# Optimization experiments

Hardware: AMD Instinct MI355X
Metric: run time of the kernel (lower is better)

Reference implementation:

```python
import jax, jax.numpy as jnp
import numpy as np

N_FFT = 2048
HOP = 441
WIN_SIZE = 7
PAD = WIN_SIZE // 2
NP_WIN = WIN_SIZE * WIN_SIZE
COV_NORM = NP_WIN / (NP_WIN - 1.0)  # sample covariance, skimage default
DATA_RANGE = 2.0  # skimage float dtype_range (-1,1)
C1 = (0.01 * DATA_RANGE) ** 2
C2 = (0.03 * DATA_RANGE) ** 2
EPS = 1e-8

# periodic hann window (librosa fftbins=True)
_HANN = 0.5 - 0.5 * np.cos(2.0 * np.pi * np.arange(N_FFT) / N_FFT)


def wav_to_spectrogram(x):
    # x: [B, C, S] -> magnitude spectrogram [B, C, T, F]
    pad = N_FFT // 2
    xp = jnp.pad(x, ((0, 0), (0, 0), (pad, pad)), mode='reflect')  # torch 'reflect'
    L = xp.shape[-1]
    n_frames = (L - N_FFT) // HOP + 1
    idx = jnp.arange(n_frames)[:, None] * HOP + jnp.arange(N_FFT)[None, :]
    frames = xp[..., idx] * jnp.asarray(_HANN, xp.dtype)  # [B,C,T,N_FFT]
    spec = jnp.fft.rfft(frames, axis=-1)
    mag = jnp.sqrt(jnp.maximum(spec.real ** 2 + spec.imag ** 2, EPS))
    return mag


def _umean_last(x):
    # 1D uniform mean filter (size 7) along last axis, scipy 'reflect' boundary
    xp = jnp.pad(x, [(0, 0)] * (x.ndim - 1) + [(PAD, PAD)], mode='symmetric')
    cs = jnp.cumsum(xp, axis=-1)
    zero = jnp.zeros(cs.shape[:-1] + (1,), cs.dtype)
    cs = jnp.concatenate([zero, cs], axis=-1)
    return (cs[..., WIN_SIZE:] - cs[..., :-WIN_SIZE]) / WIN_SIZE


def umean2d(x):
    # separable 7x7 uniform filter over last two axes
    x = _umean_last(x)
    x = jnp.swapaxes(_umean_last(jnp.swapaxes(x, -1, -2)), -1, -2)
    return x


def ssim_map_mean(X, Y):
    ux, uy = umean2d(X), umean2d(Y)
    uxx, uyy, uxy = umean2d(X * X), umean2d(Y * Y), umean2d(X * Y)
    vx = COV_NORM * (uxx - ux * ux)
    vy = COV_NORM * (uyy - uy * uy)
    vxy = COV_NORM * (uxy - ux * uy)
    S = ((2 * ux * uy + C1) * (2 * vxy + C2)) / ((ux * ux + uy * uy + C1) * (vx + vy + C2))
    # crop pad on each side (skimage) then mean over the spatial map
    return jnp.mean(S[..., PAD:-PAD, PAD:-PAD], axis=(-2, -1))


def setup_inputs() -> dict:
    key = jax.random.key(0)
    k1, k2 = jax.random.split(key)
    B, C, S = 32, 2, 176400
    output = jax.random.normal(k1, (B, C, S), dtype=jnp.float32)
    target = jax.random.normal(k2, (B, C, S), dtype=jnp.float32)
    return {"output": output, "target": target}


def reference(output, target):
    so = wav_to_spectrogram(output)
    st = wav_to_spectrogram(target)
    res = ssim_map_mean(so, st)  # [B, C]
    return res[..., None, None]  # [B, C, 1, 1]
```

## Files before the change

kernel.cpp:

```cpp
#include <hip/hip_runtime.h>
#include <math.h>

#ifndef M_PI
#define M_PI 3.14159265358979323846
#endif

constexpr int S_LEN    = 176400;
constexpr int NFFT     = 2048;
constexpr int NC       = 1024;
constexpr int HOP_     = 441;
constexpr int T_FRAMES = 401;
constexpr int F_BINS   = 1025;
constexpr int F_STRIDE = 1028;
constexpr int N_CH     = 64;
constexpr float EPS_   = 1e-8f;
constexpr float C1_    = 0.0004f;
constexpr float C2_    = 0.0036f;
constexpr float COV_NORM_ = 49.0f / 48.0f;

constexpr int WIN_OFF  = 0;
constexpr int TWG_OFF  = 2048;
constexpr int UTW_OFF  = 3584;
constexpr int SPEC_OFF = 5696;

constexpr int ROWS_PW   = 12;
constexpr int NCHUNKS_R = 33;
constexpr int BANDS     = 5;
constexpr int BAND_ADV  = 248;

typedef float vf2 __attribute__((ext_vector_type(2)));

__device__ __forceinline__ int phys(int i) { return i ^ ((i >> 2) & 15) ^ ((i >> 6) & 15); }

__device__ __forceinline__ vf2 pk_add(vf2 a, vf2 b) {
    vf2 r; asm("v_pk_add_f32 %0, %1, %2" : "=v"(r) : "v"(a), "v"(b)); return r;
}
__device__ __forceinline__ vf2 pk_sub(vf2 a, vf2 b) {
    vf2 r; asm("v_pk_add_f32 %0, %1, %2 neg_lo:[0,1] neg_hi:[0,1]" : "=v"(r) : "v"(a), "v"(b)); return r;
}
__device__ __forceinline__ vf2 pk_sub_i(vf2 b, vf2 d) {
    vf2 r; asm("v_pk_add_f32 %0, %1, %2 op_sel:[0,1] op_sel_hi:[1,0] neg_hi:[0,1]"
               : "=v"(r) : "v"(b), "v"(d)); return r;
}
__device__ __forceinline__ vf2 pk_add_i(vf2 b, vf2 d) {
    vf2 r; asm("v_pk_add_f32 %0, %1, %2 op_sel:[0,1] op_sel_hi:[1,0] neg_lo:[0,1]"
               : "=v"(r) : "v"(b), "v"(d)); return r;
}
__device__ __forceinline__ vf2 pk_cmul(vf2 y, vf2 w) {
    vf2 t, r;
    asm("v_pk_mul_f32 %0, %1, %2 op_sel:[0,0] op_sel_hi:[0,1]"
        : "=v"(t) : "v"(y), "v"(w));
    asm("v_pk_fma_f32 %0, %1, %2, %3 op_sel:[1,1,0] op_sel_hi:[1,0,1] neg_lo:[1,0,0]"
        : "=v"(r) : "v"(y), "v"(w), "v"(t));
    return r;
}

__global__ __launch_bounds__(256) void init_tables_kernel(float* __restrict__ ws, float* __restrict__ out) {
    const int idx = blockIdx.x * 256 + threadIdx.x;
    if (idx < 64) out[idx] = 0.0f;
    if (idx < NFFT) {
        ws[WIN_OFF + idx] = 0.5f - 0.5f * cosf((float)(2.0 * M_PI / NFFT) * (float)idx);
    }
    if (idx < 768) {
        float ang = -2.0f * (float)M_PI * (float)idx / (float)NC;
        float s, c; sincosf(ang, &s, &c);
        ws[TWG_OFF + 2*idx] = c; ws[TWG_OFF + 2*idx+1] = s;
    }
    if (idx < F_BINS) {
        float ang = -(float)M_PI * (float)idx / (float)NC;
        float s, c; sincosf(ang, &s, &c);
        ws[UTW_OFF + 2*idx] = c; ws[UTW_OFF + 2*idx+1] = s;
    }
}

__device__ __forceinline__ void r4_dif_inplace(
    vf2* __restrict__ A, int r0, int r1, int r2, int r3,
    vf2 w1, vf2 w2, vf2 w3, bool tw)
{
    vf2 x0c = A[r0];
    vf2 x1c = A[r1];
    vf2 x2c = A[r2];
    vf2 x3c = A[r3];

    vf2 a = pk_add(x0c, x2c);
    vf2 b = pk_sub(x0c, x2c);
    vf2 c = pk_add(x1c, x3c);
    vf2 d = pk_sub(x1c, x3c);

    vf2 y0 = pk_add(a, c);
    vf2 y2 = pk_sub(a, c);
    vf2 y1 = pk_sub_i(b, d);
    vf2 y3 = pk_add_i(b, d);

    A[r0] = y0;
    A[r1] = tw ? pk_cmul(y1, w1) : y1;
    A[r2] = tw ? pk_cmul(y2, w2) : y2;
    A[r3] = tw ? pk_cmul(y3, w3) : y3;
}

__global__ __launch_bounds__(256, 8) void stft_mag_kernel(
    const float* __restrict__ x0, const float* __restrict__ x1,
    float* __restrict__ ws, int ch0, int chbase, int nlay, int swizzle)
{
    __shared__ vf2 buf[2 * NC];

    const int tid = threadIdx.x;

    int ch, t;
    if (swizzle) {
        int g = blockIdx.x;
        ch = ch0 + (g & 7) * 8 + ((g >> 3) & 7);
        t  = g >> 6;
    } else {
        t  = blockIdx.x;
        ch = ch0 + blockIdx.y;
    }

    const float* __restrict__ xin0 = x0 + (size_t)ch * S_LEN;
    const float* __restrict__ xin1 = x1 + (size_t)ch * S_LEN;
    const float* __restrict__ win  = ws + WIN_OFF;
    const vf2*   __restrict__ twg  = (const vf2*)(ws + TWG_OFF);
    const vf2*   __restrict__ utw  = (const vf2*)(ws + UTW_OFF);

    const int base = t * HOP_ - NFFT / 2;
    float* fA0 = (float*)buf;
    float* fA1 = (float*)(buf + NC);
    if (base >= 0 && base + NFFT <= S_LEN) {
        #pragma unroll
        for (int k = 0; k < NFFT / 256; ++k) {
            int n = k * 256 + tid;
            int j = base + n;
            float w = win[n];
            int p = 2 * phys(n >> 1) + (n & 1);
            fA0[p] = xin0[j] * w;
            fA1[p] = xin1[j] * w;
        }
    } else {
        #pragma unroll
        for (int k = 0; k < NFFT / 256; ++k) {
            int n = k * 256 + tid;
            int j = base + n;
            j = (j < 0) ? -j : j;
            j = (j >= S_LEN) ? (2 * S_LEN - 2 - j) : j;
            float w = win[n];
            int p = 2 * phys(n >> 1) + (n & 1);
            fA0[p] = xin0[j] * w;
            fA1[p] = xin1[j] * w;
        }
    }
    __syncthreads();

    #pragma unroll
    for (int s = 0; s < 5; ++s) {
        const int M  = 256 >> (2 * s);
        const int q  = tid & (M - 1);
        const int e  = q << (2 * s);
        const int i0 = 4 * (tid - q) + q;

        const int r0 = phys(i0);
        const int r1 = phys(i0 + M);
        const int r2 = phys(i0 + 2 * M);
        const int r3 = phys(i0 + 3 * M);

        vf2 w1, w2, w3;
        if (s < 4) {
            w1 = twg[e];
            w2 = twg[2 * e];
            w3 = twg[3 * e];
        } else {
            w1.x = 1.0f; w1.y = 0.0f; w2 = w1; w3 = w1;
        }

        r4_dif_inplace(buf,      r0, r1, r2, r3, w1, w2, w3, s < 4);
        r4_dif_inplace(buf + NC, r0, r1, r2, r3, w1, w2, w3, s < 4);

        __syncthreads();
    }

    const size_t perT = (size_t)T_FRAMES * F_STRIDE;
    float* __restrict__ sout0 =
        ws + SPEC_OFF + (size_t)(ch - chbase) * perT + (size_t)t * F_STRIDE;
    float* __restrict__ sout1 = sout0 + (size_t)nlay * perT;

    const int R8 = ((tid & 3) << 6) | ((tid & 12) << 2) | ((tid >> 2) & 12) | ((tid >> 6) & 3);

    #pragma unroll
    for (int k = 0; k < 5; ++k) {
        int r = k * 256 + tid;
        if (k < 4 || tid == 0) {
            const int ra = (k < 4) ? ((R8 << 2) | k) : 0;
            const int rn = (NC - r) & (NC - 1);
            const int rb = ((rn & 3) << 8) | ((rn & 12) << 4) | (rn & 48)
                         | ((rn >> 4) & 12) | ((rn >> 8) & 3);
            const int ia = phys(ra);
            const int ib = phys(rb);
            vf2 wu = utw[r];

            {
                vf2 Zr = buf[ia];
                vf2 Zn = buf[ib];
                float Ex = 0.5f * (Zr.x + Zn.x);
                float Ey = 0.5f * (Zr.y - Zn.y);
                float Ox = 0.5f * (Zr.y + Zn.y);
                float Oy = 0.5f * (Zn.x - Zr.x);
                float Xx = Ex + wu.x * Ox - wu.y * Oy;
                float Xy = Ey + wu.x * Oy + wu.y * Ox;
                sout0[r] = sqrtf(fmaxf(Xx * Xx + Xy * Xy, EPS_));
            }
            {
                vf2 Zr = buf[NC + ia];
                vf2 Zn = buf[NC + ib];
                float Ex = 0.5f * (Zr.x + Zn.x);
                float Ey = 0.5f * (Zr.y - Zn.y);
                float Ox = 0.5f * (Zr.y + Zn.y);
                float Oy = 0.5f * (Zn.x - Zr.x);
                float Xx = Ex + wu.x * Ox - wu.y * Oy;
                float Xy = Ey + wu.x * Oy + wu.y * Ox;
                sout1[r] = sqrtf(fmaxf(Xx * Xx + Xy * Xy, EPS_));
            }
        }
    }
}

#define HWIN7(sarr, W) {                                                     \
    float p0 = sarr[0], p01 = p0 + sarr[1], p012 = p01 + sarr[2],            \
          P = p012 + sarr[3];                                                \
    float a1 = __shfl_down(p012, 1, 64);                                     \
    float A1 = __shfl_down(P,    1, 64);                                     \
    float b0 = __shfl_down(p0,   2, 64);                                     \
    float b1 = __shfl_down(p01,  2, 64);                                     \
    W[0] = P + a1;                                                           \
    W[1] = P - p0 + A1;                                                      \
    W[2] = W[1] - sarr[1] + b0;                                              \
    W[3] = W[2] - sarr[2] + (b1 - b0);                                       \
}

__global__ __launch_bounds__(256) void ssim_kernel(
    const float* __restrict__ ws, float* __restrict__ out,
    int ch0, int nch)
{
    const int tid  = threadIdx.x;
    const int wid  = blockIdx.x * 4 + (tid >> 6);
    const int lane = tid & 63;
    const int total = nch * BANDS * NCHUNKS_R;
    if (wid >= total) return;

    const int cg    = wid / (BANDS * NCHUNKS_R);
    const int rem   = wid - cg * (BANDS * NCHUNKS_R);
    const int band  = rem / NCHUNKS_R;
    const int chunk = rem - band * NCHUNKS_R;

    const int t0 = 3 + chunk * ROWS_PW;
    const int t1 = min(t0 + ROWS_PW, T_FRAMES - 3);

    const int cb = band * BAND_ADV;
    int c4 = cb + 4 * lane;
    if (c4 > 1024) c4 = 1024;

    const size_t perT = (size_t)T_FRAMES * F_STRIDE;
    const float* __restrict__ X = ws + SPEC_OFF + (size_t)cg * perT + c4;
    const float* __restrict__ Y = ws + SPEC_OFF + ((size_t)nch + cg) * perT + c4;

    const int  fo      = cb + 3 + 4 * lane;
    const bool lane_ok = (lane <= 61);
    const float inv49  = 1.0f / 49.0f;

    float sx[4] = {0,0,0,0}, sy[4] = {0,0,0,0}, sxx[4] = {0,0,0,0},
          syy[4] = {0,0,0,0}, sxy[4] = {0,0,0,0};
    float rgx[6][4], rgy[6][4];

    #pragma unroll
    for (int w = 0; w < 6; ++w) {
        const int rr = t0 - 3 + w;
        float4 xv = *(const float4*)(X + (size_t)rr * F_STRIDE);
        float4 yv = *(const float4*)(Y + (size_t)rr * F_STRIDE);
        float xa[4] = {xv.x, xv.y, xv.z, xv.w}, ya[4] = {yv.x, yv.y, yv.z, yv.w};
        #pragma unroll
        for (int c = 0; c < 4; ++c) {
            sx[c] += xa[c]; sy[c] += ya[c];
            sxx[c] += xa[c]*xa[c]; syy[c] += ya[c]*ya[c]; sxy[c] += xa[c]*ya[c];
            rgx[w][c] = xa[c]; rgy[w][c] = ya[c];
        }
    }

    float4 cxa = *(const float4*)(X + (size_t)(t0 + 3) * F_STRIDE);
    float4 cya = *(const float4*)(Y + (size_t)(t0 + 3) * F_STRIDE);

    double acc = 0.0;

    #pragma unroll 1
    for (int tb = t0; tb < t1; tb += 6) {
        #pragma unroll
        for (int j = 0; j < 6; ++j) {
            const int t = tb + j;
            const int tn = min(t + 4, T_FRAMES - 1);
            float4 nxa = *(const float4*)(X + (size_t)tn * F_STRIDE);
            float4 nya = *(const float4*)(Y + (size_t)tn * F_STRIDE);

            float xa[4] = {cxa.x, cxa.y, cxa.z, cxa.w};
            float ya[4] = {cya.x, cya.y, cya.z, cya.w};

            #pragma unroll
            for (int c = 0; c < 4; ++c) {
                sx[c] += xa[c]; sy[c] += ya[c];
                sxx[c] += xa[c]*xa[c]; syy[c] += ya[c]*ya[c]; sxy[c] += xa[c]*ya[c];
            }

            float wx[4], wy[4], wxx[4], wyy[4], wxy[4];
            HWIN7(sx,  wx);
            HWIN7(sy,  wy);
            HWIN7(sxx, wxx);
            HWIN7(syy, wyy);
            HWIN7(sxy, wxy);

            const bool live = (t < t1);
            #pragma unroll
            for (int c = 0; c < 4; ++c) {
                if (live && lane_ok && (fo + c <= 1021)) {
                    float ux  = wx[c]  * inv49, uy  = wy[c]  * inv49;
                    float uxx = wxx[c] * inv49, uyy = wyy[c] * inv49, uxy = wxy[c] * inv49;
                    float vx  = COV_NORM_ * (uxx - ux * ux);
                    float vy  = COV_NORM_ * (uyy - uy * uy);
                    float vxy = COV_NORM_ * (uxy - ux * uy);
                    float num = (2.f * ux * uy + C1_) * (2.f * vxy + C2_);
                    float den = (ux * ux + uy * uy + C1_) * (vx + vy + C2_);
                    acc += (double)(num * __builtin_amdgcn_rcpf(den));
                }
            }

            #pragma unroll
            for (int c = 0; c < 4; ++c) {
                float bx_ = rgx[j][c], by_ = rgy[j][c];
                sx[c]  -= bx_;      sy[c]  -= by_;
                sxx[c] -= bx_*bx_;  syy[c] -= by_*by_;  sxy[c] -= bx_*by_;
                rgx[j][c] = xa[c];  rgy[j][c] = ya[c];
            }

            cxa = nxa; cya = nya;
        }
    }

    #pragma unroll
    for (int off = 32; off > 0; off >>= 1) acc += __shfl_down(acc, off, 64);
    if (lane == 0) {
        atomicAdd(&out[ch0 + cg], (float)(acc / (395.0 * 1019.0)));
    }
}

extern "C" void kernel_launch(void* const* d_in, const int* in_sizes, int n_in,
                              void* d_out, int out_size, void* d_ws, size_t ws_size,
                              hipStream_t stream) {
    const float* x0 = (const float*)d_in[0];
    const float* x1 = (const float*)d_in[1];
    float* out = (float*)d_out;
    float* ws  = (float*)d_ws;

    const size_t table_bytes  = (size_t)SPEC_OFF * sizeof(float);
    const size_t per_ch_bytes = (size_t)2 * T_FRAMES * F_STRIDE * sizeof(float);
    int G = (int)((ws_size - table_bytes) / per_ch_bytes);
    if (G > N_CH) G = N_CH;
    if (G < 1)    G = 1;

    init_tables_kernel<<<dim3(16), dim3(256), 0, stream>>>(ws, out);

    if (G >= N_CH) {
        stft_mag_kernel<<<dim3(T_FRAMES * 64), dim3(256), 0, stream>>>(x0, x1, ws, 0, 0, N_CH, 1);
        const int nwaves = N_CH * BANDS * NCHUNKS_R;
        ssim_kernel<<<dim3((nwaves + 3) / 4), dim3(256), 0, stream>>>(ws, out, 0, N_CH);
    } else {
        for (int ch0 = 0; ch0 < N_CH; ch0 += G) {
            const int nch = (N_CH - ch0 < G) ? (N_CH - ch0) : G;
            stft_mag_kernel<<<dim3(T_FRAMES, nch), dim3(256), 0, stream>>>(x0, x1, ws, ch0, ch0, nch, 0);
            const int nwaves = nch * BANDS * NCHUNKS_R;
            ssim_kernel<<<dim3((nwaves + 3) / 4), dim3(256), 0, stream>>>(ws, out, ch0, nch);
        }
    }
}
```

Measured before the change: 374.8 us.

## Narrow SSIM lane width to 2 columns and retile rows and bands

The SSIM kernel now gives each lane 2 frequency columns instead of 4 and builds the horizontal 7-wide window from three shuffles of pair sums. Bands become narrower (9 bands of 122 columns) and each wave handles 24 rows instead of 12. The aim is lower register pressure and higher occupancy. In exchange, each column does more shuffles, neighbouring bands recompute more overlapping halo columns, and loads are narrower (float2 instead of float4).

```diff
diff --git a/kernel.cpp b/kernel.cpp
--- a/kernel.cpp
+++ b/kernel.cpp
@@ -23,10 +23,10 @@
 constexpr int UTW_OFF  = 3584;
 constexpr int SPEC_OFF = 5696;
 
-constexpr int ROWS_PW   = 12;
-constexpr int NCHUNKS_R = 33;
-constexpr int BANDS     = 5;
-constexpr int BAND_ADV  = 248;
+constexpr int ROWS_PW   = 24;
+constexpr int NCHUNKS_R = 17;
+constexpr int BANDS     = 9;
+constexpr int BAND_ADV  = 122;
 
 typedef float vf2 __attribute__((ext_vector_type(2)));
 
@@ -222,17 +222,15 @@
     }
 }
 
-#define HWIN7(sarr, W) {                                                     \
-    float p0 = sarr[0], p01 = p0 + sarr[1], p012 = p01 + sarr[2],            \
-          P = p012 + sarr[3];                                                \
-    float a1 = __shfl_down(p012, 1, 64);                                     \
-    float A1 = __shfl_down(P,    1, 64);                                     \
-    float b0 = __shfl_down(p0,   2, 64);                                     \
-    float b1 = __shfl_down(p01,  2, 64);                                     \
-    W[0] = P + a1;                                                           \
-    W[1] = P - p0 + A1;                                                      \
-    W[2] = W[1] - sarr[1] + b0;                                              \
-    W[3] = W[2] - sarr[2] + (b1 - b0);                                       \
+#define HWIN2(s, W0, W1) {                                                   \
+    float P  = (s).x + (s).y;                                                \
+    float P1 = __shfl_down(P, 1, 64);                                        \
+    float P2 = __shfl_down(P, 2, 64);                                        \
+    float P3 = __shfl_down(P, 3, 64);                                        \
+    float q3 = __shfl_down((s).x, 3, 64);                                    \
+    float Q  = P1 + P2;                                                      \
+    W0 = P + Q + q3;                                                         \
+    W1 = P - (s).x + Q + P3;                                                 \
 }
 
 __global__ __launch_bounds__(256) void ssim_kernel(
@@ -254,37 +252,34 @@
     const int t1 = min(t0 + ROWS_PW, T_FRAMES - 3);
 
     const int cb = band * BAND_ADV;
-    int c4 = cb + 4 * lane;
-    if (c4 > 1024) c4 = 1024;
+    int c2 = cb + 2 * lane;
+    if (c2 > 1026) c2 = 1026;
 
     const size_t perT = (size_t)T_FRAMES * F_STRIDE;
-    const float* __restrict__ X = ws + SPEC_OFF + (size_t)cg * perT + c4;
-    const float* __restrict__ Y = ws + SPEC_OFF + ((size_t)nch + cg) * perT + c4;
-
-    const int  fo      = cb + 3 + 4 * lane;
-    const bool lane_ok = (lane <= 61);
-    const float inv49  = 1.0f / 49.0f;
-
-    float sx[4] = {0,0,0,0}, sy[4] = {0,0,0,0}, sxx[4] = {0,0,0,0},
-          syy[4] = {0,0,0,0}, sxy[4] = {0,0,0,0};
-    float rgx[6][4], rgy[6][4];
+    const float* __restrict__ X = ws + SPEC_OFF + (size_t)cg * perT + c2;
+    const float* __restrict__ Y = ws + SPEC_OFF + ((size_t)nch + cg) * perT + c2;
+
+    const int  fo = cb + 3 + 2 * lane;
+    const bool ok = (lane <= 60);
+    const float inv49 = 1.0f / 49.0f;
+
+    float2 sx = {0,0}, sy = {0,0}, sxx = {0,0}, syy = {0,0}, sxy = {0,0};
+    float2 rgx[6], rgy[6];
 
     #pragma unroll
     for (int w = 0; w < 6; ++w) {
         const int rr = t0 - 3 + w;
-        float4 xv = *(const float4*)(X + (size_t)rr * F_STRIDE);
-        float4 yv = *(const float4*)(Y + (size_t)rr * F_STRIDE);
-        float xa[4] = {xv.x, xv.y, xv.z, xv.w}, ya[4] = {yv.x, yv.y, yv.z, yv.w};
-        #pragma unroll
-        for (int c = 0; c < 4; ++c) {
-            sx[c] += xa[c]; sy[c] += ya[c];
-            sxx[c] += xa[c]*xa[c]; syy[c] += ya[c]*ya[c]; sxy[c] += xa[c]*ya[c];
-            rgx[w][c] = xa[c]; rgy[w][c] = ya[c];
-        }
-    }
-
-    float4 cxa = *(const float4*)(X + (size_t)(t0 + 3) * F_STRIDE);
-    float4 cya = *(const float4*)(Y + (size_t)(t0 + 3) * F_STRIDE);
+        float2 xv = *(const float2*)(X + (size_t)rr * F_STRIDE);
+        float2 yv = *(const float2*)(Y + (size_t)rr * F_STRIDE);
+        sx.x += xv.x; sx.y += xv.y; sy.x += yv.x; sy.y += yv.y;
+        sxx.x += xv.x*xv.x; sxx.y += xv.y*xv.y;
+        syy.x += yv.x*yv.x; syy.y += yv.y*yv.y;
+        sxy.x += xv.x*yv.x; sxy.y += xv.y*yv.y;
+        rgx[w] = xv; rgy[w] = yv;
+    }
+
+    float2 cxa = *(const float2*)(X + (size_t)(t0 + 3) * F_STRIDE);
+    float2 cya = *(const float2*)(Y + (size_t)(t0 + 3) * F_STRIDE);
 
     double acc = 0.0;
 
@@ -294,46 +289,51 @@
         for (int j = 0; j < 6; ++j) {
             const int t = tb + j;
             const int tn = min(t + 4, T_FRAMES - 1);
-            float4 nxa = *(const float4*)(X + (size_t)tn * F_STRIDE);
-            float4 nya = *(const float4*)(Y + (size_t)tn * F_STRIDE);
-
-            float xa[4] = {cxa.x, cxa.y, cxa.z, cxa.w};
-            float ya[4] = {cya.x, cya.y, cya.z, cya.w};
-
-            #pragma unroll
-            for (int c = 0; c < 4; ++c) {
-                sx[c] += xa[c]; sy[c] += ya[c];
-                sxx[c] += xa[c]*xa[c]; syy[c] += ya[c]*ya[c]; sxy[c] += xa[c]*ya[c];
-            }
-
-            float wx[4], wy[4], wxx[4], wyy[4], wxy[4];
-            HWIN7(sx,  wx);
-            HWIN7(sy,  wy);
-            HWIN7(sxx, wxx);
-            HWIN7(syy, wyy);
-            HWIN7(sxy, wxy);
+            float2 nxa = *(const float2*)(X + (size_t)tn * F_STRIDE);
+            float2 nya = *(const float2*)(Y + (size_t)tn * F_STRIDE);
+
+            sx.x += cxa.x; sx.y += cxa.y; sy.x += cya.x; sy.y += cya.y;
+            sxx.x += cxa.x*cxa.x; sxx.y += cxa.y*cxa.y;
+            syy.x += cya.x*cya.x; syy.y += cya.y*cya.y;
+            sxy.x += cxa.x*cya.x; sxy.y += cxa.y*cya.y;
+
+            float wx0,wx1, wy0,wy1, wxx0,wxx1, wyy0,wyy1, wxy0,wxy1;
+            HWIN2(sx,  wx0,  wx1);
+            HWIN2(sy,  wy0,  wy1);
+            HWIN2(sxx, wxx0, wxx1);
+            HWIN2(syy, wyy0, wyy1);
+            HWIN2(sxy, wxy0, wxy1);
 
             const bool live = (t < t1);
-            #pragma unroll
-            for (int c = 0; c < 4; ++c) {
-                if (live && lane_ok && (fo + c <= 1021)) {
-                    float ux  = wx[c]  * inv49, uy  = wy[c]  * inv49;
-                    float uxx = wxx[c] * inv49, uyy = wyy[c] * inv49, uxy = wxy[c] * inv49;
-                    float vx  = COV_NORM_ * (uxx - ux * ux);
-                    float vy  = COV_NORM_ * (uyy - uy * uy);
-                    float vxy = COV_NORM_ * (uxy - ux * uy);
-                    float num = (2.f * ux * uy + C1_) * (2.f * vxy + C2_);
-                    float den = (ux * ux + uy * uy + C1_) * (vx + vy + C2_);
-                    acc += (double)(num * __builtin_amdgcn_rcpf(den));
-                }
-            }
-
-            #pragma unroll
-            for (int c = 0; c < 4; ++c) {
-                float bx_ = rgx[j][c], by_ = rgy[j][c];
-                sx[c]  -= bx_;      sy[c]  -= by_;
-                sxx[c] -= bx_*bx_;  syy[c] -= by_*by_;  sxy[c] -= bx_*by_;
-                rgx[j][c] = xa[c];  rgy[j][c] = ya[c];
+            if (live && ok && fo <= 1021) {
+                float ux  = wx0 * inv49, uy  = wy0 * inv49;
+                float uxx = wxx0 * inv49, uyy = wyy0 * inv49, uxy = wxy0 * inv49;
+                float vx  = COV_NORM_ * (uxx - ux * ux);
+                float vy  = COV_NORM_ * (uyy - uy * uy);
+                float vxy = COV_NORM_ * (uxy - ux * uy);
+                float num = (2.f * ux * uy + C1_) * (2.f * vxy + C2_);
+                float den = (ux * ux + uy * uy + C1_) * (vx + vy + C2_);
+                acc += (double)(num * __builtin_amdgcn_rcpf(den));
+            }
+            if (live && ok && fo + 1 <= 1021) {
+                float ux  = wx1 * inv49, uy  = wy1 * inv49;
+                float uxx = wxx1 * inv49, uyy = wyy1 * inv49, uxy = wxy1 * inv49;
+                float vx  = COV_NORM_ * (uxx - ux * ux);
+                float vy  = COV_NORM_ * (uyy - uy * uy);
+                float vxy = COV_NORM_ * (uxy - ux * uy);
+                float num = (2.f * ux * uy + C1_) * (2.f * vxy + C2_);
+                float den = (ux * ux + uy * uy + C1_) * (vx + vy + C2_);
+                acc += (double)(num * __builtin_amdgcn_rcpf(den));
+            }
+
+            {
+                float2 bx_ = rgx[j], by_ = rgy[j];
+                sx.x  -= bx_.x;      sx.y  -= bx_.y;
+                sy.x  -= by_.x;      sy.y  -= by_.y;
+                sxx.x -= bx_.x*bx_.x; sxx.y -= bx_.y*bx_.y;
+                syy.x -= by_.x*by_.x; syy.y -= by_.y*by_.y;
+                sxy.x -= bx_.x*by_.x; sxy.y -= bx_.y*by_.y;
+                rgx[j] = cxa; rgy[j] = cya;
             }
 
             cxa = nxa; cya = nya;
```

Result: faster. 364.5 us (-2.8%).
